# Kernel optimization log

Hardware: AMD Instinct MI355X
Metric: run time of the kernel (lower is better)

Reference implementation:

```python
import jax, jax.numpy as jnp
import numpy as np
import math

L, E, H, T, V, B = 8, 1024, 16, 1024, 32000, 2
HD = E // H
EPS = 1e-5


def _quantize_sym(key, shape, std=0.02):
    w = std * jax.random.normal(key, shape, jnp.float32)
    s = jnp.max(jnp.abs(w)) / 127.0  # symmetric int8: 2**(8-1)-1
    q = jnp.clip(jnp.round(w / s), -128, 127).astype(jnp.int8)
    return q, s


def setup_inputs() -> dict:
    key = jax.random.key(0)
    ks = iter(jax.random.split(key, 64 + 16 * L))
    idx = jax.random.randint(next(ks), (B, T), 0, V)
    tok_emb = 0.02 * jax.random.normal(next(ks), (V, E), jnp.float32)
    pos_emb = 0.02 * jax.random.normal(next(ks), (T, E), jnp.float32)
    # per-layer stacked params
    attn_qw, attn_s = [], []
    aproj_qw, aproj_s = [], []
    fc_qw, fc_s = [], []
    mproj_qw, mproj_s = [], []
    for _ in range(L):
        q, s = _quantize_sym(next(ks), (3 * E, E)); attn_qw.append(q); attn_s.append(s)
        q, s = _quantize_sym(next(ks), (E, E)); aproj_qw.append(q); aproj_s.append(s)
        q, s = _quantize_sym(next(ks), (4 * E, E)); fc_qw.append(q); fc_s.append(s)
        q, s = _quantize_sym(next(ks), (E, 4 * E)); mproj_qw.append(q); mproj_s.append(s)
    lm_qw, lm_s = _quantize_sym(next(ks), (V, E))
    return {
        "idx": idx,
        "tok_emb": tok_emb,
        "pos_emb": pos_emb,
        "ln1_g": jnp.ones((L, E)), "ln1_b": jnp.zeros((L, E)),
        "attn_qw": jnp.stack(attn_qw), "attn_s": jnp.stack(attn_s), "attn_b": jnp.zeros((L, 3 * E)),
        "aproj_qw": jnp.stack(aproj_qw), "aproj_s": jnp.stack(aproj_s), "aproj_b": jnp.zeros((L, E)),
        "ln2_g": jnp.ones((L, E)), "ln2_b": jnp.zeros((L, E)),
        "fc_qw": jnp.stack(fc_qw), "fc_s": jnp.stack(fc_s), "fc_b": jnp.zeros((L, 4 * E)),
        "mproj_qw": jnp.stack(mproj_qw), "mproj_s": jnp.stack(mproj_s), "mproj_b": jnp.zeros((L, E)),
        "lnf_g": jnp.ones((E,)), "lnf_b": jnp.zeros((E,)),
        "lm_qw": lm_qw, "lm_s": lm_s,
    }


def _dequant(q, s):
    return q.astype(jnp.float32) * s


def _layernorm(x, g, b):
    m = jnp.mean(x, axis=-1, keepdims=True)
    v = jnp.mean(jnp.square(x - m), axis=-1, keepdims=True)
    return (x - m) * jax.lax.rsqrt(v + EPS) * g + b


def _gpt_forward(idx, tok_emb, pos_emb, ln1_g, ln1_b, attn_qw, attn_s, attn_b,
                 aproj_qw, aproj_s, aproj_b, ln2_g, ln2_b, fc_qw, fc_s, fc_b,
                 mproj_qw, mproj_s, mproj_b, lnf_g, lnf_b, lm_qw, lm_s):
    x = tok_emb[idx] + pos_emb[None, :, :]  # [B,T,E]
    causal = jnp.tril(jnp.ones((T, T), dtype=bool))  # [T,T]
    scale = 1.0 / math.sqrt(HD)

    def block(x, p):
        (l1g, l1b, aqw, asc, ab, pqw, psc, pb,
         l2g, l2b, fqw, fsc, fb, mqw, msc, mb) = p
        h = _layernorm(x, l1g, l1b)
        qkv = h @ _dequant(aqw, asc).T + ab  # [B,T,3E]
        q, k, v = jnp.split(qkv, 3, axis=-1)
        q = q.reshape(B, T, H, HD).transpose(0, 2, 1, 3)  # [B,H,T,HD]
        k = k.reshape(B, T, H, HD).transpose(0, 2, 1, 3)
        v = v.reshape(B, T, H, HD).transpose(0, 2, 1, 3)
        att = jnp.einsum('bhqd,bhkd->bhqk', q, k) * scale
        att = jnp.where(causal, att, -jnp.inf)
        att = jax.nn.softmax(att, axis=-1)
        y = jnp.einsum('bhqk,bhkd->bhqd', att, v)
        y = y.transpose(0, 2, 1, 3).reshape(B, T, E)
        y = y @ _dequant(pqw, psc).T + pb
        x = x + y
        h = _layernorm(x, l2g, l2b)
        h = jax.nn.gelu(h @ _dequant(fqw, fsc).T + fb, approximate=False)
        x = x + h @ _dequant(mqw, msc).T + mb
        return x, None

    layer_params = (ln1_g, ln1_b, attn_qw, attn_s, attn_b,
                    aproj_qw, aproj_s, aproj_b, ln2_g, ln2_b,
                    fc_qw, fc_s, fc_b, mproj_qw, mproj_s, mproj_b)
    x, _ = jax.lax.scan(block, x, layer_params)
    x = _layernorm(x, lnf_g, lnf_b)
    logits = x @ _dequant(lm_qw, lm_s).T  # [B,T,V], no bias
    return logits


def reference(idx, tok_emb, pos_emb, ln1_g, ln1_b, attn_qw, attn_s, attn_b,
              aproj_qw, aproj_s, aproj_b, ln2_g, ln2_b, fc_qw, fc_s, fc_b,
              mproj_qw, mproj_s, mproj_b, lnf_g, lnf_b, lm_qw, lm_s):
    return _gpt_forward(idx, tok_emb, pos_emb, ln1_g, ln1_b, attn_qw, attn_s, attn_b,
                        aproj_qw, aproj_s, aproj_b, ln2_g, ln2_b, fc_qw, fc_s, fc_b,
                        mproj_qw, mproj_s, mproj_b, lnf_g, lnf_b, lm_qw, lm_s)
```

## Files before the change

kernel.cpp:

```cpp
#include <hip/hip_runtime.h>
#include <math.h>

typedef _Float16 h16;
typedef __attribute__((ext_vector_type(8))) _Float16 half8;
typedef __attribute__((ext_vector_type(4))) _Float16 half4;
typedef __attribute__((ext_vector_type(4))) float f32x4;

#define DEVI static __device__ __forceinline__

constexpr int LAY = 8, E = 1024, NH = 16, T = 1024, VOC = 32000, BATCH = 2, HD = 64;
constexpr int MROWS = BATCH * T;
constexpr int E2 = E * E;

DEVI void glds16(const void* g, void* l) {
  __builtin_amdgcn_global_load_lds((const __attribute__((address_space(1))) void*)g,
                                   (__attribute__((address_space(3))) void*)l, 16, 0, 0);
}

__global__ __launch_bounds__(256) void prep_stride_k(const unsigned char* __restrict__ qw1,
                                                     const unsigned char* __restrict__ qw2,
                                                     int* __restrict__ stridew) {
  __shared__ int red2[4], red4[4];
  const int tid = threadIdx.x;
  const int NB = 8192;
  int c2 = 0, c4 = 0;
  for (int i = tid; i < NB; i += 256) {
    const unsigned char b1 = qw1[i], b2 = qw2[i];
    const int s1 = (b1 == 0x00 || b1 == 0xFF) ? 1 : 0;
    const int s2 = (b2 == 0x00 || b2 == 0xFF) ? 1 : 0;
    if (i & 1) c2 += s1 + s2;
    if (i & 3) c4 += s1 + s2;
  }
#pragma unroll
  for (int d = 32; d >= 1; d >>= 1) { c2 += __shfl_xor(c2, d); c4 += __shfl_xor(c4, d); }
  if ((tid & 63) == 0) { red2[tid >> 6] = c2; red4[tid >> 6] = c4; }
  __syncthreads();
  if (tid == 0) {
    const int t2 = red2[0] + red2[1] + red2[2] + red2[3];
    const int t4 = red4[0] + red4[1] + red4[2] + red4[3];
    int stride = 1;
    if (t4 > (NB * 3 / 2) * 98 / 100) stride = 4;
    else if (t2 > NB * 98 / 100) stride = 2;
    stridew[0] = stride;
  }
}

DEVI half8 dq8(const signed char* src, int bstr, float s) {
  half8 o;
  if (bstr == 4) {
    int4 r0 = *reinterpret_cast<const int4*>(src);
    int4 r1 = *reinterpret_cast<const int4*>(src + 16);
    const int* c0 = reinterpret_cast<const int*>(&r0);
    const int* c1 = reinterpret_cast<const int*>(&r1);
#pragma unroll
    for (int j = 0; j < 4; ++j) o[j] = (h16)((float)c0[j] * s);
#pragma unroll
    for (int j = 0; j < 4; ++j) o[4 + j] = (h16)((float)c1[j] * s);
  } else if (bstr == 2) {
    int4 r0 = *reinterpret_cast<const int4*>(src);
    const short* c0 = reinterpret_cast<const short*>(&r0);
#pragma unroll
    for (int j = 0; j < 8; ++j) o[j] = (h16)((float)c0[j] * s);
  } else {
    int2 r0 = *reinterpret_cast<const int2*>(src);
    const signed char* c0 = reinterpret_cast<const signed char*>(&r0);
#pragma unroll
    for (int j = 0; j < 8; ++j) o[j] = (h16)((float)c0[j] * s);
  }
  return o;
}

__global__ __launch_bounds__(256) void dequant_all_k(const signed char* __restrict__ q,
                                                     const int* __restrict__ strideptr,
                                                     const float* __restrict__ sp, int P,
                                                     h16* __restrict__ out, int n) {
  const int i = (blockIdx.x * 256 + threadIdx.x) * 8;
  if (i >= n) return;
  const float s = sp[i / P];
  const int bstr = strideptr[0];
  *reinterpret_cast<half8*>(out + i) = dq8(q + (size_t)i * (size_t)bstr, bstr, s);
}

__global__ __launch_bounds__(256) void dequant_layer_k(
    const signed char* __restrict__ qkv_q, const signed char* __restrict__ ap_q,
    const signed char* __restrict__ fc_q, const signed char* __restrict__ mp_q,
    const float* __restrict__ qkv_s, const float* __restrict__ ap_s,
    const float* __restrict__ fc_s, const float* __restrict__ mp_s, int l,
    const int* __restrict__ strideptr,
    h16* __restrict__ wq, h16* __restrict__ wa, h16* __restrict__ wf,
    h16* __restrict__ wm) {
  const int e = (blockIdx.x * 256 + threadIdx.x) * 8;
  const int bstr = strideptr[0];
  const signed char* src;
  h16* dst;
  float s;
  if (e < 3 * E2) {
    src = qkv_q + ((size_t)l * 3 * E2 + e) * (size_t)bstr;
    dst = wq + e;
    s = qkv_s[l];
  } else if (e < 4 * E2) {
    const int e2 = e - 3 * E2;
    src = ap_q + ((size_t)l * E2 + e2) * (size_t)bstr;
    dst = wa + e2;
    s = ap_s[l];
  } else if (e < 8 * E2) {
    const int e2 = e - 4 * E2;
    src = fc_q + ((size_t)l * 4 * E2 + e2) * (size_t)bstr;
    dst = wf + e2;
    s = fc_s[l];
  } else {
    const int e2 = e - 8 * E2;
    src = mp_q + ((size_t)l * 4 * E2 + e2) * (size_t)bstr;
    dst = wm + e2;
    s = mp_s[l];
  }
  *reinterpret_cast<half8*>(dst) = dq8(src, bstr, s);
}

__global__ __launch_bounds__(256) void embed_k(const int* __restrict__ idx,
                                               const float* __restrict__ tok,
                                               const float* __restrict__ pos,
                                               float* __restrict__ x) {
  const int row = blockIdx.x;
  const int t = row & (T - 1);
  const int id = idx[row];
  const float4 a = reinterpret_cast<const float4*>(tok + (size_t)id * E)[threadIdx.x];
  const float4 p = reinterpret_cast<const float4*>(pos + (size_t)t * E)[threadIdx.x];
  float4 o; o.x = a.x + p.x; o.y = a.y + p.y; o.z = a.z + p.z; o.w = a.w + p.w;
  reinterpret_cast<float4*>(x + (size_t)row * E)[threadIdx.x] = o;
}

__global__ __launch_bounds__(256) void ln_k(const float* __restrict__ x,
                                            const float* __restrict__ g,
                                            const float* __restrict__ bb,
                                            h16* __restrict__ out) {
  __shared__ float red[8];
  const int row = blockIdx.x, tid = threadIdx.x;
  const float4 v = reinterpret_cast<const float4*>(x + (size_t)row * E)[tid];
  float s1 = v.x + v.y + v.z + v.w;
  float s2 = v.x * v.x + v.y * v.y + v.z * v.z + v.w * v.w;
#pragma unroll
  for (int d = 32; d >= 1; d >>= 1) { s1 += __shfl_xor(s1, d); s2 += __shfl_xor(s2, d); }
  if ((tid & 63) == 0) { red[tid >> 6] = s1; red[4 + (tid >> 6)] = s2; }
  __syncthreads();
  s1 = red[0] + red[1] + red[2] + red[3];
  s2 = red[4] + red[5] + red[6] + red[7];
  const float mean = s1 * (1.0f / E);
  const float var = s2 * (1.0f / E) - mean * mean;
  const float rstd = rsqrtf(var + 1e-5f);
  const float4 gv = reinterpret_cast<const float4*>(g)[tid];
  const float4 bv = reinterpret_cast<const float4*>(bb)[tid];
  half4 o;
  o[0] = (h16)((v.x - mean) * rstd * gv.x + bv.x);
  o[1] = (h16)((v.y - mean) * rstd * gv.y + bv.y);
  o[2] = (h16)((v.z - mean) * rstd * gv.z + bv.z);
  o[3] = (h16)((v.w - mean) * rstd * gv.w + bv.w);
  *reinterpret_cast<half4*>(out + (size_t)row * E + tid * 4) = o;
}

__global__ __launch_bounds__(256) void reduce_ln_k(const float* __restrict__ pbuf, int S,
                                                   const float* __restrict__ bias,
                                                   float* __restrict__ x,
                                                   const float* __restrict__ g,
                                                   const float* __restrict__ bb,
                                                   h16* __restrict__ out) {
  __shared__ float red[8];
  const int row = blockIdx.x, tid = threadIdx.x;
  const size_t base = (size_t)row * E + tid * 4;
  float4 a = *reinterpret_cast<const float4*>(pbuf + base);
  for (int s = 1; s < S; ++s) {
    const float4 p = *reinterpret_cast<const float4*>(pbuf + (size_t)s * MROWS * E + base);
    a.x += p.x; a.y += p.y; a.z += p.z; a.w += p.w;
  }
  const float4 bv0 = *reinterpret_cast<const float4*>(bias + tid * 4);
  float4 v = *reinterpret_cast<const float4*>(x + base);
  v.x += a.x + bv0.x; v.y += a.y + bv0.y; v.z += a.z + bv0.z; v.w += a.w + bv0.w;
  *reinterpret_cast<float4*>(x + base) = v;
  float s1 = v.x + v.y + v.z + v.w;
  float s2 = v.x * v.x + v.y * v.y + v.z * v.z + v.w * v.w;
#pragma unroll
  for (int d = 32; d >= 1; d >>= 1) { s1 += __shfl_xor(s1, d); s2 += __shfl_xor(s2, d); }
  if ((tid & 63) == 0) { red[tid >> 6] = s1; red[4 + (tid >> 6)] = s2; }
  __syncthreads();
  s1 = red[0] + red[1] + red[2] + red[3];
  s2 = red[4] + red[5] + red[6] + red[7];
  const float mean = s1 * (1.0f / E);
  const float var = s2 * (1.0f / E) - mean * mean;
  const float rstd = rsqrtf(var + 1e-5f);
  const float4 gv = *reinterpret_cast<const float4*>(g + tid * 4);
  const float4 lb = *reinterpret_cast<const float4*>(bb + tid * 4);
  half4 o;
  o[0] = (h16)((v.x - mean) * rstd * gv.x + lb.x);
  o[1] = (h16)((v.y - mean) * rstd * gv.y + lb.y);
  o[2] = (h16)((v.z - mean) * rstd * gv.z + lb.z);
  o[3] = (h16)((v.w - mean) * rstd * gv.w + lb.w);
  *reinterpret_cast<half4*>(out + (size_t)row * E + tid * 4) = o;
}

template <int OUT_KIND, int DO_GELU, int DO_RESID>
__global__ __launch_bounds__(256) void gemm_bt(const h16* __restrict__ A,
                                               const h16* __restrict__ Bw,
                                               const float* __restrict__ bias,
                                               const float* __restrict__ resid,
                                               void* __restrict__ Cout,
                                               int M, int N, int K, int ldc) {
  __shared__ __align__(16) h16 As[2][4096];
  __shared__ __align__(16) h16 Bs[2][4096];
  const int tid = threadIdx.x;
  const int w = tid >> 6, lane = tid & 63;
  const int lin = blockIdx.x;
  const int cpx = gridDim.x >> 3;
  const int swz = (lin & 7) * cpx + (lin >> 3);
  const int m0 = (swz & 15) << 7;
  const int n0 = (swz >> 4) << 7;
  const int wr = w >> 1, wc = w & 1;
  const int lr = lane >> 2, lc8 = (lane & 3) << 3;
  const h16* gA = A + (size_t)(m0 + w * 16 + lr) * K + lc8;
  const h16* gB = Bw + (size_t)(n0 + w * 16 + lr) * K + lc8;
  f32x4 acc[4][4] = {};
  const int fl = lane & 15, fk = (lane >> 4) << 3;
  const int nk = K >> 5;
  auto stage = [&](int buf, int kt) {
    const h16* pa = gA + (kt << 5);
    const h16* pb = gB + (kt << 5);
    glds16(pa, &As[buf][w * 512]);
    glds16(pa + (size_t)64 * K, &As[buf][2048 + w * 512]);
    glds16(pb, &Bs[buf][w * 512]);
    glds16(pb + (size_t)64 * K, &Bs[buf][2048 + w * 512]);
  };
  stage(0, 0);
  __syncthreads();
  int cur = 0;
  for (int kt = 0; kt < nk; ++kt) {
    if (kt + 1 < nk) stage(cur ^ 1, kt + 1);
    half8 af[4], bfr[4];
#pragma unroll
    for (int mi = 0; mi < 4; ++mi)
      af[mi] = *reinterpret_cast<const half8*>(&As[cur][(wr * 64 + mi * 16 + fl) * 32 + fk]);
#pragma unroll
    for (int ni = 0; ni < 4; ++ni)
      bfr[ni] = *reinterpret_cast<const half8*>(&Bs[cur][(wc * 64 + ni * 16 + fl) * 32 + fk]);
#pragma unroll
    for (int mi = 0; mi < 4; ++mi)
#pragma unroll
      for (int ni = 0; ni < 4; ++ni)
        acc[mi][ni] = __builtin_amdgcn_mfma_f32_16x16x32_f16(af[mi], bfr[ni], acc[mi][ni], 0, 0, 0);
    __syncthreads();
    cur ^= 1;
  }
  const int fr4 = (lane >> 4) << 2;
#pragma unroll
  for (int mi = 0; mi < 4; ++mi) {
#pragma unroll
    for (int ni = 0; ni < 4; ++ni) {
      const int col = n0 + wc * 64 + ni * 16 + fl;
      const float bv = bias ? bias[col] : 0.0f;
#pragma unroll
      for (int j = 0; j < 4; ++j) {
        const int row = m0 + wr * 64 + mi * 16 + fr4 + j;
        float v = acc[mi][ni][j] + bv;
        if (DO_GELU) v = 0.5f * v * (1.0f + erff(v * 0.70710678118f));
        if (DO_RESID) v += resid[(size_t)row * ldc + col];
        if (OUT_KIND == 1)
          reinterpret_cast<h16*>(Cout)[(size_t)row * ldc + col] = (h16)v;
        else
          reinterpret_cast<float*>(Cout)[(size_t)row * ldc + col] = v;
      }
    }
  }
}

__global__ __launch_bounds__(512) void gemm_bt256(const h16* __restrict__ A,
                                                  const h16* __restrict__ Bw,
                                                  float* __restrict__ Cout,
                                                  int M, int N, int K) {
  __shared__ __align__(16) h16 As[2][8192];
  __shared__ __align__(16) h16 Bs[2][8192];
  const int tid = threadIdx.x;
  const int w = tid >> 6, lane = tid & 63;
  const int lin = blockIdx.x;
  const int cpx = gridDim.x >> 3;
  const int swz = (lin & 7) * cpx + (lin >> 3);
  const int m0 = (swz & 7) << 8;
  const int n0 = (swz >> 3) << 8;
  const int wr = w >> 2, wc = w & 3;
  const int lr = lane >> 2, lc8 = (lane & 3) << 3;
  const h16* gA = A + (size_t)(m0 + w * 16 + lr) * K + lc8;
  const h16* gB = Bw + (size_t)(n0 + w * 16 + lr) * K + lc8;
  f32x4 acc[8][4] = {};
  const int fl = lane & 15, fk = (lane >> 4) << 3;
  const int nk = K >> 5;
  auto stage = [&](int buf, int kt) {
    const h16* pa = gA + (kt << 5);
    const h16* pb = gB + (kt << 5);
    glds16(pa, &As[buf][w * 512]);
    glds16(pa + (size_t)128 * K, &As[buf][4096 + w * 512]);
    glds16(pb, &Bs[buf][w * 512]);
    glds16(pb + (size_t)128 * K, &Bs[buf][4096 + w * 512]);
  };
  stage(0, 0);
  __syncthreads();
  int cur = 0;
  for (int kt = 0; kt < nk; ++kt) {
    if (kt + 1 < nk) stage(cur ^ 1, kt + 1);
    half8 af[8], bfr[4];
#pragma unroll
    for (int mi = 0; mi < 8; ++mi)
      af[mi] = *reinterpret_cast<const half8*>(&As[cur][(wr * 128 + mi * 16 + fl) * 32 + fk]);
#pragma unroll
    for (int ni = 0; ni < 4; ++ni)
      bfr[ni] = *reinterpret_cast<const half8*>(&Bs[cur][(wc * 64 + ni * 16 + fl) * 32 + fk]);
#pragma unroll
    for (int mi = 0; mi < 8; ++mi)
#pragma unroll
      for (int ni = 0; ni < 4; ++ni)
        acc[mi][ni] = __builtin_amdgcn_mfma_f32_16x16x32_f16(af[mi], bfr[ni], acc[mi][ni], 0, 0, 0);
    __syncthreads();
    cur ^= 1;
  }
  const int fr4 = (lane >> 4) << 2;
#pragma unroll
  for (int mi = 0; mi < 8; ++mi)
#pragma unroll
    for (int ni = 0; ni < 4; ++ni) {
      const int col = n0 + wc * 64 + ni * 16 + fl;
#pragma unroll
      for (int j = 0; j < 4; ++j) {
        const int row = m0 + wr * 128 + mi * 16 + fr4 + j;
        Cout[(size_t)row * N + col] = acc[mi][ni][j];
      }
    }
}

__global__ __launch_bounds__(256) void gemm_btk(const h16* __restrict__ A,
                                                const h16* __restrict__ Bw,
                                                float* __restrict__ pbuf,
                                                int M, int N, int Kc, int ldk) {
  __shared__ __align__(16) h16 As[2][4096];
  __shared__ __align__(16) h16 Bs[2][4096];
  const int tid = threadIdx.x;
  const int w = tid >> 6, lane = tid & 63;
  const int lin = blockIdx.x;
  const int cpx = gridDim.x >> 3;
  const int swz = (lin & 7) * cpx + (lin >> 3);
  const int m0 = (swz & 15) << 7;
  const int n0 = (swz >> 4) << 7;
  const int s = blockIdx.y;
  const int koff = s * Kc;
  const int wr = w >> 1, wc = w & 1;
  const int lr = lane >> 2, lc8 = (lane & 3) << 3;
  const h16* gA = A + (size_t)(m0 + w * 16 + lr) * ldk + koff + lc8;
  const h16* gB = Bw + (size_t)(n0 + w * 16 + lr) * ldk + koff + lc8;
  f32x4 acc[4][4] = {};
  const int fl = lane & 15, fk = (lane >> 4) << 3;
  const int nk = Kc >> 5;
  auto stage = [&](int buf, int kt) {
    const h16* pa = gA + (kt << 5);
    const h16* pb = gB + (kt << 5);
    glds16(pa, &As[buf][w * 512]);
    glds16(pa + (size_t)64 * ldk, &As[buf][2048 + w * 512]);
    glds16(pb, &Bs[buf][w * 512]);
    glds16(pb + (size_t)64 * ldk, &Bs[buf][2048 + w * 512]);
  };
  stage(0, 0);
  __syncthreads();
  int cur = 0;
  for (int kt = 0; kt < nk; ++kt) {
    if (kt + 1 < nk) stage(cur ^ 1, kt + 1);
    half8 af[4], bfr[4];
#pragma unroll
    for (int mi = 0; mi < 4; ++mi)
      af[mi] = *reinterpret_cast<const half8*>(&As[cur][(wr * 64 + mi * 16 + fl) * 32 + fk]);
#pragma unroll
    for (int ni = 0; ni < 4; ++ni)
      bfr[ni] = *reinterpret_cast<const half8*>(&Bs[cur][(wc * 64 + ni * 16 + fl) * 32 + fk]);
#pragma unroll
    for (int mi = 0; mi < 4; ++mi)
#pragma unroll
      for (int ni = 0; ni < 4; ++ni)
        acc[mi][ni] = __builtin_amdgcn_mfma_f32_16x16x32_f16(af[mi], bfr[ni], acc[mi][ni], 0, 0, 0);
    __syncthreads();
    cur ^= 1;
  }
  float* out = pbuf + (size_t)s * M * N;
  const int fr4 = (lane >> 4) << 2;
#pragma unroll
  for (int mi = 0; mi < 4; ++mi)
#pragma unroll
    for (int ni = 0; ni < 4; ++ni) {
      const int col = n0 + wc * 64 + ni * 16 + fl;
#pragma unroll
      for (int j = 0; j < 4; ++j) {
        const int row = m0 + wr * 64 + mi * 16 + fr4 + j;
        out[(size_t)row * N + col] = acc[mi][ni][j];
      }
    }
}

__global__ __launch_bounds__(256) void attn_k(const h16* __restrict__ qkv,
                                              h16* __restrict__ yout) {
  __shared__ __align__(16) h16 Ks[4096];
  __shared__ __align__(16) h16 VTs[4096];
  __shared__ __align__(16) h16 Ps[4096];
  const int qt = blockIdx.x, bh = blockIdx.y;
  const int b = bh >> 4, h = bh & 15;
  const int tid = threadIdx.x, w = tid >> 6, lane = tid & 63;
  const int fl = lane & 15, fkg = lane >> 4, fk = fkg << 3;
  const size_t rowQ0 = (size_t)b * T + qt * 64 + w * 16;
  const h16* qbase = qkv + (rowQ0 + fl) * 3072 + h * 64;
  const half8 qf0 = *reinterpret_cast<const half8*>(qbase + fk);
  const half8 qf1 = *reinterpret_cast<const half8*>(qbase + 32 + fk);
  f32x4 yacc[4] = {};
  float m_run[4], l_run[4];
#pragma unroll
  for (int j = 0; j < 4; ++j) { m_run[j] = -1e30f; l_run[j] = 0.f; }
  const int q_g0 = qt * 64 + w * 16 + (fkg << 2);
  const int krow = lane >> 3, kcol8 = (lane & 7) << 3;
  const int vrow = tid >> 2, vcol8 = (tid & 3) << 3;
  for (int kt = 0; kt <= qt; ++kt) {
    __syncthreads();
    const size_t kbase = (size_t)b * T + kt * 64;
    const h16* gk = qkv + (kbase + w * 8 + krow) * 3072 + E + h * 64 + kcol8;
    glds16(gk, &Ks[w * 512]);
    glds16(gk + (size_t)32 * 3072, &Ks[2048 + w * 512]);
    {
      const h16* gv = qkv + (kbase + vrow) * 3072 + 2 * E + h * 64 + vcol8;
      const half8 v0 = *reinterpret_cast<const half8*>(gv);
      const half8 v1 = *reinterpret_cast<const half8*>(gv + 32);
#pragma unroll
      for (int e = 0; e < 8; ++e) VTs[(vcol8 + e) * 64 + vrow] = v0[e];
#pragma unroll
      for (int e = 0; e < 8; ++e) VTs[(vcol8 + 32 + e) * 64 + vrow] = v1[e];
    }
    __syncthreads();
    f32x4 sacc[4];
#pragma unroll
    for (int ni = 0; ni < 4; ++ni) {
      const half8 kb0 = *reinterpret_cast<const half8*>(&Ks[(ni * 16 + fl) * 64 + fk]);
      const half8 kb1 = *reinterpret_cast<const half8*>(&Ks[(ni * 16 + fl) * 64 + 32 + fk]);
      f32x4 z = {0.f, 0.f, 0.f, 0.f};
      z = __builtin_amdgcn_mfma_f32_16x16x32_f16(qf0, kb0, z, 0, 0, 0);
      z = __builtin_amdgcn_mfma_f32_16x16x32_f16(qf1, kb1, z, 0, 0, 0);
      sacc[ni] = z;
    }
    float tmax[4] = {-1e30f, -1e30f, -1e30f, -1e30f};
#pragma unroll
    for (int ni = 0; ni < 4; ++ni) {
      const int kcol = kt * 64 + ni * 16 + fl;
#pragma unroll
      for (int j = 0; j < 4; ++j) {
        float sv = sacc[ni][j] * 0.125f;
        sv = (kcol > q_g0 + j) ? -1e30f : sv;
        sacc[ni][j] = sv;
        tmax[j] = fmaxf(tmax[j], sv);
      }
    }
#pragma unroll
    for (int d = 1; d < 16; d <<= 1) {
#pragma unroll
      for (int j = 0; j < 4; ++j) tmax[j] = fmaxf(tmax[j], __shfl_xor(tmax[j], d));
    }
    float sc_old[4], psum[4] = {0.f, 0.f, 0.f, 0.f};
#pragma unroll
    for (int j = 0; j < 4; ++j) {
      const float mn = fmaxf(m_run[j], tmax[j]);
      sc_old[j] = __expf(m_run[j] - mn);
      m_run[j] = mn;
    }
#pragma unroll
    for (int ni = 0; ni < 4; ++ni)
#pragma unroll
      for (int j = 0; j < 4; ++j) {
        const float p = __expf(sacc[ni][j] - m_run[j]);
        sacc[ni][j] = p;
        psum[j] += p;
      }
#pragma unroll
    for (int d = 1; d < 16; d <<= 1) {
#pragma unroll
      for (int j = 0; j < 4; ++j) psum[j] += __shfl_xor(psum[j], d);
    }
#pragma unroll
    for (int j = 0; j < 4; ++j) l_run[j] = l_run[j] * sc_old[j] + psum[j];
#pragma unroll
    for (int di = 0; di < 4; ++di)
#pragma unroll
      for (int j = 0; j < 4; ++j) yacc[di][j] *= sc_old[j];
#pragma unroll
    for (int ni = 0; ni < 4; ++ni)
#pragma unroll
      for (int j = 0; j < 4; ++j)
        Ps[w * 1024 + ((fkg << 2) + j) * 64 + ni * 16 + fl] = (h16)sacc[ni][j];
    __syncthreads();
    const half8 pa0 = *reinterpret_cast<const half8*>(&Ps[w * 1024 + fl * 64 + fk]);
    const half8 pa1 = *reinterpret_cast<const half8*>(&Ps[w * 1024 + fl * 64 + 32 + fk]);
#pragma unroll
    for (int di = 0; di < 4; ++di) {
      const half8 vb0 = *reinterpret_cast<const half8*>(&VTs[(di * 16 + fl) * 64 + fk]);
      const half8 vb1 = *reinterpret_cast<const half8*>(&VTs[(di * 16 + fl) * 64 + 32 + fk]);
      yacc[di] = __builtin_amdgcn_mfma_f32_16x16x32_f16(pa0, vb0, yacc[di], 0, 0, 0);
      yacc[di] = __builtin_amdgcn_mfma_f32_16x16x32_f16(pa1, vb1, yacc[di], 0, 0, 0);
    }
  }
  float rl[4];
#pragma unroll
  for (int j = 0; j < 4; ++j) rl[j] = 1.0f / l_run[j];
  const size_t orow0 = rowQ0 + (fkg << 2);
#pragma unroll
  for (int di = 0; di < 4; ++di)
#pragma unroll
    for (int j = 0; j < 4; ++j)
      yout[(orow0 + j) * E + h * 64 + di * 16 + fl] = (h16)(yacc[di][j] * rl[j]);
}

extern "C" void kernel_launch(void* const* d_in, const int* in_sizes, int n_in,
                              void* d_out, int out_size, void* d_ws, size_t ws_size,
                              hipStream_t stream) {
  (void)in_sizes; (void)n_in; (void)out_size; (void)ws_size;
  const int* idx = (const int*)d_in[0];
  const float* tok = (const float*)d_in[1];
  const float* pos = (const float*)d_in[2];
  const float* ln1g = (const float*)d_in[3];
  const float* ln1b = (const float*)d_in[4];
  const signed char* attn_qw = (const signed char*)d_in[5];
  const float* attn_s = (const float*)d_in[6];
  const float* attn_b = (const float*)d_in[7];
  const signed char* aproj_qw = (const signed char*)d_in[8];
  const float* aproj_s = (const float*)d_in[9];
  const float* aproj_b = (const float*)d_in[10];
  const float* ln2g = (const float*)d_in[11];
  const float* ln2b = (const float*)d_in[12];
  const signed char* fc_qw = (const signed char*)d_in[13];
  const float* fc_s = (const float*)d_in[14];
  const float* fc_b = (const float*)d_in[15];
  const signed char* mproj_qw = (const signed char*)d_in[16];
  const float* mproj_s = (const float*)d_in[17];
  const float* mproj_b = (const float*)d_in[18];
  const float* lnfg = (const float*)d_in[19];
  const float* lnfb = (const float*)d_in[20];
  const signed char* lm_qw = (const signed char*)d_in[21];
  const float* lm_s = (const float*)d_in[22];

  char* ws = (char*)d_ws;
  size_t off = 0;
  auto alloc = [&](size_t bytes) {
    char* p = ws + off;
    off += (bytes + 255) & ~(size_t)255;
    return p;
  };
  float* x = (float*)alloc((size_t)MROWS * E * 4);
  h16* hbuf = (h16*)alloc((size_t)MROWS * E * 2);
  h16* big = (h16*)alloc((size_t)MROWS * 4 * E * 2);
  h16* wq = (h16*)alloc((size_t)3 * E2 * 2);
  h16* wa = (h16*)alloc((size_t)E2 * 2);
  h16* wf = (h16*)alloc((size_t)4 * E2 * 2);
  h16* wm = (h16*)alloc((size_t)4 * E2 * 2);
  float* pbuf = (float*)alloc((size_t)4 * MROWS * E * 4);
  h16* wlm = (h16*)alloc((size_t)VOC * E * 2);
  int* stridew = (int*)alloc(256);
  h16* qkvb = big;
  h16* yb = hbuf;
  h16* hfc = big;

  prep_stride_k<<<1, 256, 0, stream>>>((const unsigned char*)attn_qw,
                                       (const unsigned char*)fc_qw, stridew);
  dequant_all_k<<<VOC * E / 2048, 256, 0, stream>>>(lm_qw, stridew, lm_s, VOC * E,
                                                    wlm, VOC * E);
  embed_k<<<MROWS, 256, 0, stream>>>(idx, tok, pos, x);
  ln_k<<<MROWS, 256, 0, stream>>>(x, ln1g, ln1b, hbuf);

  for (int l = 0; l < LAY; ++l) {
    dequant_layer_k<<<12 * E2 / 2048, 256, 0, stream>>>(
        attn_qw, aproj_qw, fc_qw, mproj_qw, attn_s, aproj_s, fc_s, mproj_s, l,
        stridew, wq, wa, wf, wm);
    gemm_bt<1, 0, 0><<<24 * 16, 256, 0, stream>>>(hbuf, wq, attn_b + l * 3 * E, nullptr,
                                                  qkvb, MROWS, 3 * E, E, 3 * E);
    attn_k<<<dim3(16, 32), 256, 0, stream>>>(qkvb, yb);
    gemm_btk<<<dim3(128, 2), 256, 0, stream>>>(yb, wa, pbuf, MROWS, E, 512, E);
    reduce_ln_k<<<MROWS, 256, 0, stream>>>(pbuf, 2, aproj_b + l * E, x,
                                           ln2g + l * E, ln2b + l * E, hbuf);
    gemm_bt<1, 1, 0><<<32 * 16, 256, 0, stream>>>(hbuf, wf, fc_b + l * 4 * E, nullptr,
                                                  hfc, MROWS, 4 * E, E, 4 * E);
    gemm_btk<<<dim3(128, 4), 256, 0, stream>>>(hfc, wm, pbuf, MROWS, E, 1024, 4 * E);
    const float* ng = (l < LAY - 1) ? (ln1g + (l + 1) * E) : lnfg;
    const float* nb = (l < LAY - 1) ? (ln1b + (l + 1) * E) : lnfb;
    reduce_ln_k<<<MROWS, 256, 0, stream>>>(pbuf, 4, mproj_b + l * E, x, ng, nb, hbuf);
  }
  gemm_bt256<<<1000, 512, 0, stream>>>(hbuf, wlm, (float*)d_out, MROWS, VOC, E);
}
```

Before: 1.828 ms.

## Double-buffer K/V tiles in attention and schedule longest causal tiles first

The attention kernel now keeps two shared-memory buffers for K and transposed V. It issues the next tile's K async copy and V global loads before computing on the current tile, and scatters V into the alternate buffer mid-iteration. This overlaps global-memory latency with MFMA and softmax work. Query tiles are also processed in reverse order so the heaviest causal blocks start first, improving load balance. The cost is double the LDS for K/V, which may reduce occupancy, plus extra registers for the prefetched V.

```diff
diff --git a/kernel.cpp b/kernel.cpp
--- a/kernel.cpp
+++ b/kernel.cpp
@@ -399,10 +399,11 @@
 
 __global__ __launch_bounds__(256) void attn_k(const h16* __restrict__ qkv,
                                               h16* __restrict__ yout) {
-  __shared__ __align__(16) h16 Ks[4096];
-  __shared__ __align__(16) h16 VTs[4096];
+  __shared__ __align__(16) h16 Ks[2][4096];
+  __shared__ __align__(16) h16 VTs[2][4096];
   __shared__ __align__(16) h16 Ps[4096];
-  const int qt = blockIdx.x, bh = blockIdx.y;
+  const int qt = (int)gridDim.x - 1 - (int)blockIdx.x;
+  const int bh = blockIdx.y;
   const int b = bh >> 4, h = bh & 15;
   const int tid = threadIdx.x, w = tid >> 6, lane = tid & 63;
   const int fl = lane & 15, fkg = lane >> 4, fk = fkg << 3;
@@ -417,27 +418,45 @@
   const int q_g0 = qt * 64 + w * 16 + (fkg << 2);
   const int krow = lane >> 3, kcol8 = (lane & 7) << 3;
   const int vrow = tid >> 2, vcol8 = (tid & 3) << 3;
-  for (int kt = 0; kt <= qt; ++kt) {
-    __syncthreads();
+
+  auto stageK = [&](int kt, int buf) {
     const size_t kbase = (size_t)b * T + kt * 64;
     const h16* gk = qkv + (kbase + w * 8 + krow) * 3072 + E + h * 64 + kcol8;
-    glds16(gk, &Ks[w * 512]);
-    glds16(gk + (size_t)32 * 3072, &Ks[2048 + w * 512]);
-    {
-      const h16* gv = qkv + (kbase + vrow) * 3072 + 2 * E + h * 64 + vcol8;
-      const half8 v0 = *reinterpret_cast<const half8*>(gv);
-      const half8 v1 = *reinterpret_cast<const half8*>(gv + 32);
-#pragma unroll
-      for (int e = 0; e < 8; ++e) VTs[(vcol8 + e) * 64 + vrow] = v0[e];
-#pragma unroll
-      for (int e = 0; e < 8; ++e) VTs[(vcol8 + 32 + e) * 64 + vrow] = v1[e];
-    }
-    __syncthreads();
+    glds16(gk, &Ks[buf][w * 512]);
+    glds16(gk + (size_t)32 * 3072, &Ks[buf][2048 + w * 512]);
+  };
+  auto loadV = [&](int kt, int half32) {
+    const size_t kbase = (size_t)b * T + kt * 64;
+    return *reinterpret_cast<const half8*>(qkv + (kbase + vrow) * 3072 + 2 * E + h * 64 +
+                                           vcol8 + half32);
+  };
+  auto scatterV = [&](int buf, half8 v0, half8 v1) {
+#pragma unroll
+    for (int e = 0; e < 8; ++e) VTs[buf][(vcol8 + e) * 64 + vrow] = v0[e];
+#pragma unroll
+    for (int e = 0; e < 8; ++e) VTs[buf][(vcol8 + 32 + e) * 64 + vrow] = v1[e];
+  };
+
+  stageK(0, 0);
+  {
+    half8 v0 = loadV(0, 0), v1 = loadV(0, 32);
+    scatterV(0, v0, v1);
+  }
+  __syncthreads();
+  int cur = 0;
+  for (int kt = 0; kt <= qt; ++kt) {
+    const bool hn = kt < qt;
+    half8 nv0, nv1;
+    if (hn) {
+      stageK(kt + 1, cur ^ 1);
+      nv0 = loadV(kt + 1, 0);
+      nv1 = loadV(kt + 1, 32);
+    }
     f32x4 sacc[4];
 #pragma unroll
     for (int ni = 0; ni < 4; ++ni) {
-      const half8 kb0 = *reinterpret_cast<const half8*>(&Ks[(ni * 16 + fl) * 64 + fk]);
-      const half8 kb1 = *reinterpret_cast<const half8*>(&Ks[(ni * 16 + fl) * 64 + 32 + fk]);
+      const half8 kb0 = *reinterpret_cast<const half8*>(&Ks[cur][(ni * 16 + fl) * 64 + fk]);
+      const half8 kb1 = *reinterpret_cast<const half8*>(&Ks[cur][(ni * 16 + fl) * 64 + 32 + fk]);
       f32x4 z = {0.f, 0.f, 0.f, 0.f};
       z = __builtin_amdgcn_mfma_f32_16x16x32_f16(qf0, kb0, z, 0, 0, 0);
       z = __builtin_amdgcn_mfma_f32_16x16x32_f16(qf1, kb1, z, 0, 0, 0);
@@ -486,6 +505,7 @@
     for (int di = 0; di < 4; ++di)
 #pragma unroll
       for (int j = 0; j < 4; ++j) yacc[di][j] *= sc_old[j];
+    if (hn) scatterV(cur ^ 1, nv0, nv1);
 #pragma unroll
     for (int ni = 0; ni < 4; ++ni)
 #pragma unroll
@@ -496,11 +516,13 @@
     const half8 pa1 = *reinterpret_cast<const half8*>(&Ps[w * 1024 + fl * 64 + 32 + fk]);
 #pragma unroll
     for (int di = 0; di < 4; ++di) {
-      const half8 vb0 = *reinterpret_cast<const half8*>(&VTs[(di * 16 + fl) * 64 + fk]);
-      const half8 vb1 = *reinterpret_cast<const half8*>(&VTs[(di * 16 + fl) * 64 + 32 + fk]);
+      const half8 vb0 = *reinterpret_cast<const half8*>(&VTs[cur][(di * 16 + fl) * 64 + fk]);
+      const half8 vb1 = *reinterpret_cast<const half8*>(&VTs[cur][(di * 16 + fl) * 64 + 32 + fk]);
       yacc[di] = __builtin_amdgcn_mfma_f32_16x16x32_f16(pa0, vb0, yacc[di], 0, 0, 0);
       yacc[di] = __builtin_amdgcn_mfma_f32_16x16x32_f16(pa1, vb1, yacc[di], 0, 0, 0);
     }
+    __syncthreads();
+    cur ^= 1;
   }
   float rl[4];
 #pragma unroll
```

After: 1.807 ms. About the same (-1.1%).
